# Kernel optimization log

Hardware: AMD Instinct MI355X
Metric: run time of the kernel (lower is better)

## Reference

```python
import jax, jax.numpy as jnp
import numpy as np

N_NODES = 100000
N_EDGES = 3200000
D_IN = 256
H1 = 16
H2 = 32


def _xavier(key, shape):
    fan_in, fan_out = shape
    a = jnp.sqrt(6.0 / (fan_in + fan_out))
    return jax.random.uniform(key, shape, jnp.float32, -a, a)


def setup_inputs() -> dict:
    key = jax.random.key(0)
    ks = jax.random.split(key, 8)
    x = jax.random.normal(ks[0], (N_NODES, D_IN), jnp.float32)
    edge_rows = jax.random.randint(ks[1], (N_EDGES,), 0, N_NODES, jnp.int32)
    edge_cols = jax.random.randint(ks[2], (N_EDGES,), 0, N_NODES, jnp.int32)
    edge_vals = jax.random.uniform(ks[3], (N_EDGES,), jnp.float32)
    W1 = _xavier(ks[4], (D_IN, H1))
    W2 = _xavier(ks[5], (H1, H2))
    w_out = _xavier(ks[6], (H2, 1))
    b_out = jnp.zeros((1,), jnp.float32)
    return {"x": x, "edge_vals": edge_vals, "W1": W1, "W2": W2,
            "w_out": w_out, "b_out": b_out,
            "edge_rows": edge_rows, "edge_cols": edge_cols}


def _spmm(edge_rows, edge_cols, edge_vals, dense):
    # out[i] = sum_{e: row[e]==i} val[e] * dense[col[e]]  == torch.spmm(adj, dense)
    gathered = dense[edge_cols] * edge_vals[:, None]  # [E, F]
    return jax.ops.segment_sum(gathered, edge_rows, num_segments=N_NODES)


def reference(x, edge_vals, W1, W2, w_out, b_out, edge_rows, edge_cols):
    # gc1: mm -> spmm -> relu (dropout=0)
    h = jax.nn.relu(_spmm(edge_rows, edge_cols, edge_vals, x @ W1))  # [N, H1]
    # gc2: mm -> spmm -> identity
    z = _spmm(edge_rows, edge_cols, edge_vals, h @ W2)  # [N, H2]
    z_pooled = jnp.sum(z, axis=0)  # [H2]
    out = jax.nn.sigmoid(z_pooled @ w_out + b_out)  # [1]
    return out
```

## Files before the change

### kernel.cpp

```cpp
#include <hip/hip_runtime.h>
#include <math.h>

#define N_NODES 100000
#define D_IN 256
#define H1 16
#define H2 32

static __device__ __forceinline__ float bf_lo(unsigned int u) {
    return __uint_as_float(u << 16);
}
static __device__ __forceinline__ float bf_hi(unsigned int u) {
    return __uint_as_float(u & 0xffff0000u);
}
static __device__ __forceinline__ unsigned int f2bf_rne(float f) {
    unsigned int u = __float_as_uint(f);
    return (u + 0x7fffu + ((u >> 16) & 1u)) >> 16;
}
static __device__ __forceinline__ unsigned int pack_bf16(float lo, float hi) {
    return f2bf_rne(lo) | (f2bf_rne(hi) << 16);
}
static __device__ __forceinline__ unsigned int cvt_pk_bf16(float lo, float hi) {
    unsigned int r;
    asm("v_cvt_pk_bf16_f32 %0, %1, %2" : "=v"(r) : "v"(lo), "v"(hi));
    return r;
}

typedef __attribute__((ext_vector_type(8))) short bf16x8;
typedef __attribute__((ext_vector_type(4))) float f32x4;
union ABFrag { unsigned int u[4]; bf16x8 v; };

__global__ void k_zero(float4* __restrict__ p, int n4) {
    int i = blockIdx.x * blockDim.x + threadIdx.x;
    if (i < n4) p[i] = make_float4(0.f, 0.f, 0.f, 0.f);
}

#define XW1_TILES 2
#define XW1_ROWS (4 * XW1_TILES * 16)
__global__ __launch_bounds__(256) void k_xw1(const float* __restrict__ x,
                                             const float* __restrict__ W1,
                                             unsigned short* __restrict__ t,
                                             int n_nodes) {
    const int lane = threadIdx.x & 63;
    const int wid  = threadIdx.x >> 6;
    const int fcol = lane & 15;
    const int kgrp = lane >> 4;

    ABFrag bfrag[8];
#pragma unroll
    for (int g = 0; g < 8; g++) {
        const float* wp = W1 + (g * 32 + kgrp * 8) * H1 + fcol;
#pragma unroll
        for (int p = 0; p < 4; p++)
            bfrag[g].u[p] = cvt_pk_bf16(wp[(2 * p) * H1], wp[(2 * p + 1) * H1]);
    }

    const int wrow0 = blockIdx.x * XW1_ROWS + wid * (XW1_TILES * 16);
#pragma unroll
    for (int tile = 0; tile < XW1_TILES; tile++) {
        const int row0 = wrow0 + tile * 16;
        int arow = row0 + fcol;
        if (arow >= n_nodes) arow = n_nodes - 1;
        const float* xr = x + (size_t)arow * D_IN;
        f32x4 acc = {0.f, 0.f, 0.f, 0.f};
#pragma unroll
        for (int g = 0; g < 8; g++) {
            const float4 a0 = *(const float4*)(xr + g * 32 + kgrp * 8);
            const float4 a1 = *(const float4*)(xr + g * 32 + kgrp * 8 + 4);
            ABFrag af;
            af.u[0] = cvt_pk_bf16(a0.x, a0.y);
            af.u[1] = cvt_pk_bf16(a0.z, a0.w);
            af.u[2] = cvt_pk_bf16(a1.x, a1.y);
            af.u[3] = cvt_pk_bf16(a1.z, a1.w);
            acc = __builtin_amdgcn_mfma_f32_16x16x32_bf16(af.v, bfrag[g].v, acc, 0, 0, 0);
        }
#pragma unroll
        for (int r = 0; r < 4; r++) {
            int orow = row0 + kgrp * 4 + r;
            if (orow < n_nodes)
                t[(size_t)orow * H1 + fcol] = (unsigned short)f2bf_rne(acc[r]);
        }
    }
}

__global__ __launch_bounds__(256) void k_edge(const int* __restrict__ rows,
                                              const int* __restrict__ cols,
                                              const float* __restrict__ vals,
                                              const unsigned int* __restrict__ tb,
                                              unsigned int* __restrict__ g2,
                                              int E) {
    int tid = blockIdx.x * 256 + threadIdx.x;
    int e = tid >> 3;
    int f2 = tid & 7;
    if (e >= E) return;
    int r = rows[e];
    int c = cols[e];
    float v = vals[e];
    unsigned int tv = tb[c * 8 + f2];
    unsigned int pk = pack_bf16(v * bf_lo(tv), v * bf_hi(tv));
    unsigned int* addr = g2 + (r * 8 + f2);
    asm volatile("global_atomic_pk_add_bf16 %0, %1, off"
                 :: "v"(addr), "v"(pk) : "memory");
}

__global__ __launch_bounds__(256) void k_s2(const int* __restrict__ cols,
                                            const float* __restrict__ vals,
                                            const unsigned int* __restrict__ g2,
                                            float* __restrict__ s,
                                            int E) {
    const int f2 = threadIdx.x & 7;
    int idx    = (blockIdx.x * 256 + threadIdx.x) >> 3;
    int stride = (gridDim.x * 256) >> 3;
    float accl = 0.f, acch = 0.f;
    for (int e = idx; e < E; e += stride) {
        int c = cols[e];
        float v = vals[e];
        unsigned int gv = g2[c * 8 + f2];
        accl = fmaf(v, fmaxf(bf_lo(gv), 0.f), accl);
        acch = fmaf(v, fmaxf(bf_hi(gv), 0.f), acch);
    }
    accl += __shfl_xor(accl, 8, 64);
    accl += __shfl_xor(accl, 16, 64);
    accl += __shfl_xor(accl, 32, 64);
    acch += __shfl_xor(acch, 8, 64);
    acch += __shfl_xor(acch, 16, 64);
    acch += __shfl_xor(acch, 32, 64);
    __shared__ float red[4][16];
    int lane = threadIdx.x & 63, wid = threadIdx.x >> 6;
    if (lane < 8) { red[wid][2 * lane] = accl; red[wid][2 * lane + 1] = acch; }
    __syncthreads();
    if (threadIdx.x < 16) {
        float v = red[0][threadIdx.x] + red[1][threadIdx.x] +
                  red[2][threadIdx.x] + red[3][threadIdx.x];
        atomicAdd(&s[threadIdx.x], v);
    }
}

__global__ void k_out(const float* __restrict__ s, const float* __restrict__ W2,
                      const float* __restrict__ w_out,
                      const float* __restrict__ b_out,
                      float* __restrict__ out) {
    int f2 = threadIdx.x;
    float m = 0.f;
    if (f2 < H2) {
        float v = 0.f;
#pragma unroll
        for (int f1 = 0; f1 < H1; f1++) v = fmaf(s[f1], W2[f1 * H2 + f2], v);
        m = v * w_out[f2];
    }
    for (int off = 32; off; off >>= 1) m += __shfl_down(m, off, 64);
    if (f2 == 0) out[0] = 1.f / (1.f + expf(-(m + b_out[0])));
}

extern "C" void kernel_launch(void* const* d_in, const int* in_sizes, int n_in,
                              void* d_out, int out_size, void* d_ws, size_t ws_size,
                              hipStream_t stream) {
    const float* x         = (const float*)d_in[0];
    const float* edge_vals = (const float*)d_in[1];
    const float* W1        = (const float*)d_in[2];
    const float* W2        = (const float*)d_in[3];
    const float* w_out     = (const float*)d_in[4];
    const float* b_out     = (const float*)d_in[5];
    const int*   edge_rows = (const int*)d_in[6];
    const int*   edge_cols = (const int*)d_in[7];
    float* out = (float*)d_out;

    const int N = N_NODES;
    const int E = in_sizes[1];

    char* ws = (char*)d_ws;
    unsigned int*   g2 = (unsigned int*)(ws);
    float*          s  = (float*)(ws + 3200000);
    unsigned short* t  = (unsigned short*)(ws + 3200064);

    const int n4 = 200004;
    k_zero<<<(n4 + 255) / 256, 256, 0, stream>>>((float4*)ws, n4);

    k_xw1<<<(N + XW1_ROWS - 1) / XW1_ROWS, 256, 0, stream>>>(x, W1, t, N);

    long long edge_threads = (long long)E * 8;
    k_edge<<<(int)((edge_threads + 255) / 256), 256, 0, stream>>>(
        edge_rows, edge_cols, edge_vals, (const unsigned int*)t, g2, E);

    k_s2<<<1024, 256, 0, stream>>>(edge_cols, edge_vals, g2, s, E);

    k_out<<<1, 64, 0, stream>>>(s, W2, w_out, b_out, out);
}
```

Measured before the change: 405.3 us.

## Bin edges by destination row block and accumulate in shared memory

Replaces the per-edge global bf16 atomic scatter with a counting-sort pipeline. A histogram pass counts edges per 128-row bucket, a scan turns the counts into offsets, and a scatter pass packs edges into buckets. A per-bucket kernel then accumulates rows in LDS with fp32 atomics and writes bf16 results. The aim is to remove contended global atomics and the precision loss from bf16 atomic adds, at the cost of several extra passes over the edge arrays and a large workspace. The binned path is only taken when the workspace is big enough.

```diff
diff --git a/kernel.cpp b/kernel.cpp
--- a/kernel.cpp
+++ b/kernel.cpp
@@ -5,6 +5,10 @@
 #define D_IN 256
 #define H1 16
 #define H2 32
+#define BSHIFT 7
+#define NB 782
+#define CH 8192
+#define HIST_BLOCKS 160
 
 static __device__ __forceinline__ float bf_lo(unsigned int u) {
     return __uint_as_float(u << 16);
@@ -82,12 +86,114 @@
     }
 }
 
+__global__ __launch_bounds__(256) void k_hist(const int* __restrict__ rows,
+                                              int* __restrict__ hist, int E) {
+    __shared__ int lh[NB];
+    int tid = threadIdx.x;
+    for (int b = tid; b < NB; b += 256) lh[b] = 0;
+    __syncthreads();
+    int stride = gridDim.x * 256;
+    for (int i = blockIdx.x * 256 + tid; i < E; i += stride)
+        atomicAdd(&lh[rows[i] >> BSHIFT], 1);
+    __syncthreads();
+    for (int b = tid; b < NB; b += 256) {
+        int c = lh[b];
+        if (c) atomicAdd(&hist[b], c);
+    }
+}
+
+__global__ __launch_bounds__(1024) void k_scan(const int* __restrict__ hist,
+                                               int* __restrict__ base,
+                                               unsigned int* __restrict__ cursor) {
+    __shared__ int sa[1024], sb[1024];
+    int tid = threadIdx.x;
+    int h0 = (tid < NB) ? hist[tid] : 0;
+    sa[tid] = h0;
+    __syncthreads();
+    int* src = sa; int* dst = sb;
+    for (int off = 1; off < 1024; off <<= 1) {
+        int v = src[tid];
+        if (tid >= off) v += src[tid - off];
+        dst[tid] = v;
+        __syncthreads();
+        int* tmp = src; src = dst; dst = tmp;
+    }
+    int incl = src[tid];
+    if (tid < NB) {
+        int excl = incl - h0;
+        base[tid] = excl;
+        cursor[tid * 16] = (unsigned int)excl;
+    }
+    if (tid == NB - 1) base[NB] = incl;
+}
+
+__global__ __launch_bounds__(256) void k_scatter(const int* __restrict__ rows,
+                                                 const int* __restrict__ cols,
+                                                 const float* __restrict__ vals,
+                                                 unsigned int* __restrict__ cursor,
+                                                 uint2* __restrict__ ed, int E) {
+    __shared__ int lcount[NB];
+    __shared__ int lbase[NB];
+    int tid = threadIdx.x;
+    int c0 = blockIdx.x * CH;
+    int cend = min(c0 + CH, E);
+    for (int b = tid; b < NB; b += 256) lcount[b] = 0;
+    __syncthreads();
+    for (int i = c0 + tid; i < cend; i += 256)
+        atomicAdd(&lcount[rows[i] >> BSHIFT], 1);
+    __syncthreads();
+    for (int b = tid; b < NB; b += 256) {
+        int cnt = lcount[b];
+        lbase[b] = cnt ? (int)atomicAdd(&cursor[b * 16], (unsigned int)cnt) : 0;
+        lcount[b] = 0;
+    }
+    __syncthreads();
+    for (int i = c0 + tid; i < cend; i += 256) {
+        int r = rows[i];
+        int b = r >> BSHIFT;
+        int rank = atomicAdd(&lcount[b], 1);
+        int pos = lbase[b] + rank;
+        ed[pos] = make_uint2(((unsigned int)cols[i] << BSHIFT) | (unsigned int)(r & 127),
+                             __float_as_uint(vals[i]));
+    }
+}
+
+__global__ __launch_bounds__(256) void k_gacc(const uint2* __restrict__ ed,
+                                              const int* __restrict__ base,
+                                              const unsigned short* __restrict__ t,
+                                              unsigned int* __restrict__ g2,
+                                              int n_nodes) {
+    __shared__ float gs[128 * H1];
+    int tid = threadIdx.x;
+    int b = blockIdx.x;
+    for (int i = tid; i < 128 * H1; i += 256) gs[i] = 0.f;
+    __syncthreads();
+    int e0 = base[b], e1 = base[b + 1];
+    int f = tid & 15, grp = tid >> 4;
+    for (int i = e0 + grp; i < e1; i += 16) {
+        uint2 e = ed[i];
+        int c = (int)(e.x >> BSHIFT);
+        int r7 = (int)(e.x & 127);
+        float v = __uint_as_float(e.y);
+        float tv = __uint_as_float((unsigned int)t[c * H1 + f] << 16);
+        atomicAdd(&gs[r7 * H1 + f], v * tv);
+    }
+    __syncthreads();
+    int row0 = b << BSHIFT;
+    for (int j = tid; j < 128 * H1 / 2; j += 256) {
+        int row = j >> 3, fp = j & 7;
+        int grow = row0 + row;
+        if (grow < n_nodes)
+            g2[grow * 8 + fp] = pack_bf16(gs[row * H1 + 2 * fp],
+                                          gs[row * H1 + 2 * fp + 1]);
+    }
+}
+
 __global__ __launch_bounds__(256) void k_edge(const int* __restrict__ rows,
                                               const int* __restrict__ cols,
                                               const float* __restrict__ vals,
                                               const unsigned int* __restrict__ tb,
-                                              unsigned int* __restrict__ g2,
-                                              int E) {
+                                              unsigned int* __restrict__ g2, int E) {
     int tid = blockIdx.x * 256 + threadIdx.x;
     int e = tid >> 3;
     int f2 = tid & 7;
@@ -105,8 +211,7 @@
 __global__ __launch_bounds__(256) void k_s2(const int* __restrict__ cols,
                                             const float* __restrict__ vals,
                                             const unsigned int* __restrict__ g2,
-                                            float* __restrict__ s,
-                                            int E) {
+                                            float* __restrict__ s, int E) {
     const int f2 = threadIdx.x & 7;
     int idx    = (blockIdx.x * 256 + threadIdx.x) >> 3;
     int stride = (gridDim.x * 256) >> 3;
@@ -168,18 +273,32 @@
     const int E = in_sizes[1];
 
     char* ws = (char*)d_ws;
-    unsigned int*   g2 = (unsigned int*)(ws);
-    float*          s  = (float*)(ws + 3200000);
-    unsigned short* t  = (unsigned short*)(ws + 3200064);
-
-    const int n4 = 200004;
-    k_zero<<<(n4 + 255) / 256, 256, 0, stream>>>((float4*)ws, n4);
+    unsigned short* t    = (unsigned short*)(ws);
+    unsigned int*   g2   = (unsigned int*)(ws + 3200000);
+    float*          s    = (float*)(ws + 6400000);
+    int*            hist = (int*)(ws + 6400064);
+    int*            base = (int*)(ws + 6403200);
+    unsigned int*   cur  = (unsigned int*)(ws + 6406400);
+    uint2*          ed   = (uint2*)(ws + 6456448);
+
+    bool binned = (ws_size >= 32100000);
 
     k_xw1<<<(N + XW1_ROWS - 1) / XW1_ROWS, 256, 0, stream>>>(x, W1, t, N);
 
-    long long edge_threads = (long long)E * 8;
-    k_edge<<<(int)((edge_threads + 255) / 256), 256, 0, stream>>>(
-        edge_rows, edge_cols, edge_vals, (const unsigned int*)t, g2, E);
+    if (binned) {
+        k_zero<<<1, 256, 0, stream>>>((float4*)(ws + 6400000), 200);
+        k_hist<<<HIST_BLOCKS, 256, 0, stream>>>(edge_rows, hist, E);
+        k_scan<<<1, 1024, 0, stream>>>(hist, base, cur);
+        k_scatter<<<(E + CH - 1) / CH, 256, 0, stream>>>(
+            edge_rows, edge_cols, edge_vals, cur, ed, E);
+        k_gacc<<<NB, 256, 0, stream>>>(ed, base, t, g2, N);
+    } else {
+        k_zero<<<(200004 + 255) / 256, 256, 0, stream>>>(
+            (float4*)(ws + 3200000), 200004);
+        long long edge_threads = (long long)E * 8;
+        k_edge<<<(int)((edge_threads + 255) / 256), 256, 0, stream>>>(
+            edge_rows, edge_cols, edge_vals, (const unsigned int*)t, g2, E);
+    }
 
     k_s2<<<1024, 256, 0, stream>>>(edge_cols, edge_vals, g2, s, E);
 
```

Result: slower. 717.8 us (+77.1%).

## Replace atomic edge scatter with cooperative bucket sort and shared-memory aggregation

Applied to the files above, without the earlier changes.

Merges the whole pipeline into one cooperative kernel with grid syncs. Edges are bucketed by destination row block using a histogram, a prefix scan and a scatter, and the first SpMM then accumulates each 64-row block in shared memory before writing bf16 output, with no global atomics. The histogram also runs alongside the X·W1 matmul on separate blocks. The cost is extra passes over the edge arrays (histogram, scatter), a 25 MB edge buffer, several grid-wide barriers, and serial single-block scan latency.

```diff
diff --git a/kernel.cpp b/kernel.cpp
--- a/kernel.cpp
+++ b/kernel.cpp
@@ -1,10 +1,19 @@
 #include <hip/hip_runtime.h>
+#include <hip/hip_cooperative_groups.h>
 #include <math.h>
+
+namespace cg = cooperative_groups;
 
 #define N_NODES 100000
 #define D_IN 256
 #define H1 16
 #define H2 32
+#define BSHIFT 6
+#define BROWS 64
+#define NB 1563
+#define NT1 782
+#define HB 160
+#define CH 8192
 
 static __device__ __forceinline__ float bf_lo(unsigned int u) {
     return __uint_as_float(u << 16);
@@ -29,19 +38,12 @@
 typedef __attribute__((ext_vector_type(4))) float f32x4;
 union ABFrag { unsigned int u[4]; bf16x8 v; };
 
-__global__ void k_zero(float4* __restrict__ p, int n4) {
-    int i = blockIdx.x * blockDim.x + threadIdx.x;
-    if (i < n4) p[i] = make_float4(0.f, 0.f, 0.f, 0.f);
-}
-
-#define XW1_TILES 2
-#define XW1_ROWS (4 * XW1_TILES * 16)
-__global__ __launch_bounds__(256) void k_xw1(const float* __restrict__ x,
-                                             const float* __restrict__ W1,
-                                             unsigned short* __restrict__ t,
-                                             int n_nodes) {
-    const int lane = threadIdx.x & 63;
-    const int wid  = threadIdx.x >> 6;
+static __device__ __forceinline__ void xw1_block(const float* __restrict__ x,
+                                                 const float* __restrict__ W1,
+                                                 unsigned short* __restrict__ t,
+                                                 int tt, int tid) {
+    const int lane = tid & 63;
+    const int wid  = tid >> 6;
     const int fcol = lane & 15;
     const int kgrp = lane >> 4;
 
@@ -54,12 +56,12 @@
             bfrag[g].u[p] = cvt_pk_bf16(wp[(2 * p) * H1], wp[(2 * p + 1) * H1]);
     }
 
-    const int wrow0 = blockIdx.x * XW1_ROWS + wid * (XW1_TILES * 16);
-#pragma unroll
-    for (int tile = 0; tile < XW1_TILES; tile++) {
+    const int wrow0 = tt * 128 + wid * 32;
+#pragma unroll
+    for (int tile = 0; tile < 2; tile++) {
         const int row0 = wrow0 + tile * 16;
         int arow = row0 + fcol;
-        if (arow >= n_nodes) arow = n_nodes - 1;
+        if (arow >= N_NODES) arow = N_NODES - 1;
         const float* xr = x + (size_t)arow * D_IN;
         f32x4 acc = {0.f, 0.f, 0.f, 0.f};
 #pragma unroll
@@ -76,18 +78,205 @@
 #pragma unroll
         for (int r = 0; r < 4; r++) {
             int orow = row0 + kgrp * 4 + r;
-            if (orow < n_nodes)
+            if (orow < N_NODES)
                 t[(size_t)orow * H1 + fcol] = (unsigned short)f2bf_rne(acc[r]);
         }
     }
+}
+
+union MegaSmem {
+    int lh[NB];
+    struct { int lcount[NB]; int lbase[NB]; } sc;
+    float gs[BROWS * H1];
+    int scan[256];
+    float red[4][16];
+};
+
+__global__ __launch_bounds__(256, 4) void k_mega(
+    const float* __restrict__ x, const float* __restrict__ edge_vals,
+    const float* __restrict__ W1, const float* __restrict__ W2,
+    const float* __restrict__ w_out, const float* __restrict__ b_out,
+    const int* __restrict__ edge_rows, const int* __restrict__ edge_cols,
+    float* __restrict__ out,
+    unsigned short* __restrict__ t, unsigned int* __restrict__ g2,
+    float* __restrict__ s, int* __restrict__ base, int* __restrict__ hist,
+    unsigned int* __restrict__ cursor, int* __restrict__ hist_priv,
+    uint2* __restrict__ ed, int E)
+{
+    cg::grid_group grid = cg::this_grid();
+    const int tid = threadIdx.x;
+    const int bid = blockIdx.x;
+    const int G   = gridDim.x;
+    __shared__ MegaSmem sm;
+
+    if (bid == 0 && tid < 16) s[tid] = 0.f;
+    if (bid < HB) {
+        for (int b = tid; b < NB; b += 256) sm.lh[b] = 0;
+        __syncthreads();
+        for (int i = bid * 256 + tid; i < E; i += HB * 256)
+            atomicAdd(&sm.lh[edge_rows[i] >> BSHIFT], 1);
+        __syncthreads();
+        for (int b = tid; b < NB; b += 256) hist_priv[bid * NB + b] = sm.lh[b];
+    } else {
+        for (int tt = bid - HB; tt < NT1; tt += (G - HB))
+            xw1_block(x, W1, t, tt, tid);
+    }
+    __threadfence(); grid.sync(); __threadfence();
+
+    for (int b = bid * 256 + tid; b < NB; b += G * 256) {
+        int sum = 0;
+#pragma unroll 4
+        for (int p = 0; p < HB; p++) sum += hist_priv[p * NB + b];
+        hist[b] = sum;
+    }
+    __threadfence(); grid.sync(); __threadfence();
+
+    if (bid == 0) {
+        int loc[7]; int mysum = 0;
+#pragma unroll
+        for (int j = 0; j < 7; j++) {
+            int b = tid * 7 + j;
+            int h = (b < NB) ? hist[b] : 0;
+            loc[j] = mysum; mysum += h;
+        }
+        sm.scan[tid] = mysum;
+        __syncthreads();
+        int incl = mysum;
+        for (int off = 1; off < 256; off <<= 1) {
+            int add = (tid >= off) ? sm.scan[tid - off] : 0;
+            __syncthreads();
+            incl += add; sm.scan[tid] = incl;
+            __syncthreads();
+        }
+        int excl = incl - mysum;
+#pragma unroll
+        for (int j = 0; j < 7; j++) {
+            int b = tid * 7 + j;
+            if (b < NB) {
+                int v = excl + loc[j];
+                base[b] = v;
+                cursor[b * 8] = (unsigned int)v;
+            }
+        }
+        if (tid == 255) base[NB] = incl;
+    }
+    __threadfence(); grid.sync(); __threadfence();
+
+    const int nch = (E + CH - 1) / CH;
+    for (int ch = bid; ch < nch; ch += G) {
+        const int c0 = ch * CH;
+        const int c1 = min(c0 + CH, E);
+        for (int b = tid; b < NB; b += 256) sm.sc.lcount[b] = 0;
+        __syncthreads();
+        for (int i = c0 + tid; i < c1; i += 256)
+            atomicAdd(&sm.sc.lcount[edge_rows[i] >> BSHIFT], 1);
+        __syncthreads();
+        for (int b = tid; b < NB; b += 256) {
+            int c = sm.sc.lcount[b];
+            sm.sc.lbase[b] = c ? (int)atomicAdd(&cursor[b * 8], (unsigned int)c) : 0;
+            sm.sc.lcount[b] = 0;
+        }
+        __syncthreads();
+        for (int i = c0 + tid; i < c1; i += 256) {
+            int r = edge_rows[i];
+            int b = r >> BSHIFT;
+            int rank = atomicAdd(&sm.sc.lcount[b], 1);
+            int pos = sm.sc.lbase[b] + rank;
+            ed[pos] = make_uint2(((unsigned int)edge_cols[i] << BSHIFT) |
+                                     (unsigned int)(r & (BROWS - 1)),
+                                 __float_as_uint(edge_vals[i]));
+        }
+        __syncthreads();
+    }
+    __threadfence(); grid.sync(); __threadfence();
+
+    const unsigned int* tp = (const unsigned int*)t;
+    for (int b = bid; b < NB; b += G) {
+        for (int i = tid; i < BROWS * H1; i += 256) sm.gs[i] = 0.f;
+        __syncthreads();
+        const int e0 = base[b], e1 = base[b + 1];
+        const int f2 = tid & 7, grp = tid >> 3;
+        for (int i = e0 + grp; i < e1; i += 32) {
+            uint2 e = ed[i];
+            int c  = (int)(e.x >> BSHIFT);
+            int r6 = (int)(e.x & (BROWS - 1));
+            float v = __uint_as_float(e.y);
+            unsigned int tv = tp[c * 8 + f2];
+            atomicAdd(&sm.gs[r6 * H1 + 2 * f2],     v * bf_lo(tv));
+            atomicAdd(&sm.gs[r6 * H1 + 2 * f2 + 1], v * bf_hi(tv));
+        }
+        __syncthreads();
+        const int row0 = b << BSHIFT;
+        for (int j = tid; j < BROWS * H1 / 2; j += 256) {
+            int row = j >> 3, fp = j & 7;
+            int grow = row0 + row;
+            if (grow < N_NODES)
+                g2[grow * 8 + fp] = pack_bf16(sm.gs[row * H1 + 2 * fp],
+                                              sm.gs[row * H1 + 2 * fp + 1]);
+        }
+        __syncthreads();
+    }
+    __threadfence(); grid.sync(); __threadfence();
+
+    {
+        const int f2 = tid & 7;
+        int idx    = (bid * 256 + tid) >> 3;
+        int stride = G * 32;
+        float accl = 0.f, acch = 0.f;
+        for (int e = idx; e < E; e += stride) {
+            int c = edge_cols[e];
+            float v = edge_vals[e];
+            unsigned int gv = g2[c * 8 + f2];
+            accl = fmaf(v, fmaxf(bf_lo(gv), 0.f), accl);
+            acch = fmaf(v, fmaxf(bf_hi(gv), 0.f), acch);
+        }
+        accl += __shfl_xor(accl, 8, 64);
+        accl += __shfl_xor(accl, 16, 64);
+        accl += __shfl_xor(accl, 32, 64);
+        acch += __shfl_xor(acch, 8, 64);
+        acch += __shfl_xor(acch, 16, 64);
+        acch += __shfl_xor(acch, 32, 64);
+        int lane = tid & 63, wid = tid >> 6;
+        __syncthreads();
+        if (lane < 8) { sm.red[wid][2 * lane] = accl; sm.red[wid][2 * lane + 1] = acch; }
+        __syncthreads();
+        if (tid < 16) {
+            float v = sm.red[0][tid] + sm.red[1][tid] + sm.red[2][tid] + sm.red[3][tid];
+            atomicAdd(&s[tid], v);
+        }
+    }
+    __threadfence(); grid.sync(); __threadfence();
+
+    if (bid == 0 && tid < 64) {
+        int f2 = tid;
+        float m = 0.f;
+        if (f2 < H2) {
+            float v = 0.f;
+#pragma unroll
+            for (int f1 = 0; f1 < H1; f1++) v = fmaf(s[f1], W2[f1 * H2 + f2], v);
+            m = v * w_out[f2];
+        }
+        for (int off = 32; off; off >>= 1) m += __shfl_down(m, off, 64);
+        if (f2 == 0) out[0] = 1.f / (1.f + expf(-(m + b_out[0])));
+    }
+}
+
+__global__ void k_zero(float4* __restrict__ p, int n4) {
+    int i = blockIdx.x * blockDim.x + threadIdx.x;
+    if (i < n4) p[i] = make_float4(0.f, 0.f, 0.f, 0.f);
+}
+
+__global__ __launch_bounds__(256) void k_xw1(const float* __restrict__ x,
+                                             const float* __restrict__ W1,
+                                             unsigned short* __restrict__ t) {
+    xw1_block(x, W1, t, blockIdx.x, threadIdx.x);
 }
 
 __global__ __launch_bounds__(256) void k_edge(const int* __restrict__ rows,
                                               const int* __restrict__ cols,
                                               const float* __restrict__ vals,
                                               const unsigned int* __restrict__ tb,
-                                              unsigned int* __restrict__ g2,
-                                              int E) {
+                                              unsigned int* __restrict__ g2, int E) {
     int tid = blockIdx.x * 256 + threadIdx.x;
     int e = tid >> 3;
     int f2 = tid & 7;
@@ -105,8 +294,7 @@
 __global__ __launch_bounds__(256) void k_s2(const int* __restrict__ cols,
                                             const float* __restrict__ vals,
                                             const unsigned int* __restrict__ g2,
-                                            float* __restrict__ s,
-                                            int E) {
+                                            float* __restrict__ s, int E) {
     const int f2 = threadIdx.x & 7;
     int idx    = (blockIdx.x * 256 + threadIdx.x) >> 3;
     int stride = (gridDim.x * 256) >> 3;
@@ -164,24 +352,55 @@
     const int*   edge_cols = (const int*)d_in[7];
     float* out = (float*)d_out;
 
-    const int N = N_NODES;
     const int E = in_sizes[1];
 
     char* ws = (char*)d_ws;
-    unsigned int*   g2 = (unsigned int*)(ws);
-    float*          s  = (float*)(ws + 3200000);
-    unsigned short* t  = (unsigned short*)(ws + 3200064);
-
-    const int n4 = 200004;
-    k_zero<<<(n4 + 255) / 256, 256, 0, stream>>>((float4*)ws, n4);
-
-    k_xw1<<<(N + XW1_ROWS - 1) / XW1_ROWS, 256, 0, stream>>>(x, W1, t, N);
-
-    long long edge_threads = (long long)E * 8;
-    k_edge<<<(int)((edge_threads + 255) / 256), 256, 0, stream>>>(
-        edge_rows, edge_cols, edge_vals, (const unsigned int*)t, g2, E);
-
-    k_s2<<<1024, 256, 0, stream>>>(edge_cols, edge_vals, g2, s, E);
-
-    k_out<<<1, 64, 0, stream>>>(s, W2, w_out, b_out, out);
-}
+    unsigned short* t    = (unsigned short*)(ws);
+    unsigned int*   g2   = (unsigned int*)(ws + 3200000);
+    float*          s    = (float*)(ws + 6400000);
+    int*            base = (int*)(ws + 6400064);
+    int*            hist = (int*)(ws + 6406336);
+    unsigned int*   cur  = (unsigned int*)(ws + 6412608);
+    int*            hp   = (int*)(ws + 6462656);
+    uint2*          ed   = (uint2*)(ws + 7463040);
+
+    bool mega_ok = (ws_size >= 33100000) && (E <= 3200000);
+    if (mega_ok) {
+        static int grid_blocks = 0;
+        if (grid_blocks == 0) {
+            int maxb = 0;
+            if (hipOccupancyMaxActiveBlocksPerMultiprocessor(
+                    &maxb, (const void*)k_mega, 256, 0) != hipSuccess || maxb < 1)
+                maxb = 2;
+            int ncu = 256, dev = 0;
+            hipDeviceProp_t prop;
+            if (hipGetDevice(&dev) == hipSuccess &&
+                hipGetDeviceProperties(&prop, dev) == hipSuccess)
+                ncu = prop.multiProcessorCount;
+            grid_blocks = maxb * ncu;
+            if (grid_blocks > 2048) grid_blocks = 2048;
+            if (grid_blocks < 256)  grid_blocks = 256;
+        }
+        void* args[] = {(void*)&x, (void*)&edge_vals, (void*)&W1, (void*)&W2,
+                        (void*)&w_out, (void*)&b_out, (void*)&edge_rows,
+                        (void*)&edge_cols, (void*)&out, (void*)&t, (void*)&g2,
+                        (void*)&s, (void*)&base, (void*)&hist, (void*)&cur,
+                        (void*)&hp, (void*)&ed, (void*)&E};
+        hipError_t err = hipLaunchCooperativeKernel(
+            (const void*)k_mega, dim3(grid_blocks), dim3(256), args, 0, stream);
+        if (err != hipSuccess) mega_ok = false;
+    }
+
+    if (!mega_ok) {
+        unsigned int*   fg2 = (unsigned int*)(ws);
+        float*          fs  = (float*)(ws + 3200000);
+        unsigned short* ft  = (unsigned short*)(ws + 3200064);
+        k_zero<<<(200004 + 255) / 256, 256, 0, stream>>>((float4*)ws, 200004);
+        k_xw1<<<NT1, 256, 0, stream>>>(x, W1, ft);
+        long long edge_threads = (long long)E * 8;
+        k_edge<<<(int)((edge_threads + 255) / 256), 256, 0, stream>>>(
+            edge_rows, edge_cols, edge_vals, (const unsigned int*)ft, fg2, E);
+        k_s2<<<1024, 256, 0, stream>>>(edge_cols, edge_vals, fg2, fs, E);
+        k_out<<<1, 64, 0, stream>>>(fs, W2, w_out, b_out, out);
+    }
+}
```

Measured after the change: 1.517 ms. 274% more time.
